# Performance work log

Hardware: AMD Instinct MI355X
Metric: run time of the kernel (lower is better)

## Reference

```python
import jax, jax.numpy as jnp
import numpy as np

H = 8          # n_heads
MRF = 128      # max_rf random features
EPS = 1e-4


def fiber2head(feats, h):
    # feats: list of [N, m_d, 2d+1] -> [N, h, sum_d (m_d/h)*(2d+1)]
    N = feats[0].shape[0]
    return jnp.concatenate([f.reshape(N, h, -1) for f in feats], axis=-1)


def softmax_kernel(data, w, is_query):
    # FAVOR+ positive random features. data: [B,H,L,d], w: [m,d]
    dn = data.shape[-1] ** -0.25
    ratio = w.shape[0] ** -0.5
    dd = jnp.einsum('bhld,md->bhlm', data * dn, w)
    diag = (data * data).sum(-1, keepdims=True) * (0.5 * dn * dn)
    if is_query:
        mx = jax.lax.stop_gradient(dd.max(-1, keepdims=True))
    else:
        mx = jax.lax.stop_gradient(dd.max())
    return ratio * (jnp.exp(dd - diag - mx) + EPS)


def setup_inputs() -> dict:
    key = jax.random.key(0)
    ks = jax.random.split(key, 7)
    B, L = 4, 8192
    N = B * L
    v0 = jax.random.normal(ks[0], (N, 64, 1), jnp.float32)
    v1 = jax.random.normal(ks[1], (N, 64, 3), jnp.float32)
    k0 = jax.random.normal(ks[2], (N, 64, 1), jnp.float32)
    k1 = jax.random.normal(ks[3], (N, 64, 3), jnp.float32)
    q0 = jax.random.normal(ks[4], (N, 64, 1), jnp.float32)
    q1 = jax.random.normal(ks[5], (N, 64, 3), jnp.float32)
    w = jax.random.normal(ks[6], (MRF, 32), jnp.float32)  # random-feature projection
    return {'v0': v0, 'v1': v1, 'k0': k0, 'k1': k1, 'q0': q0, 'q1': q1, 'w': w, 'batch_size': 4}


def reference(v0, v1, k0, k1, q0, q1, w, batch_size):
    B = batch_size
    N = v0.shape[0]
    L = N // B
    # Q from the k-dict (as in source); source then overwrites K with Q, so the
    # q-dict features are mathematically unused.
    Q = fiber2head([k0, k1], H).reshape(B, L, H, -1).transpose(0, 2, 1, 3)  # [B,H,L,d_k]
    K = Q  # faithful to `K = Q.view(...)` in the source
    Kp = softmax_kernel(K, w, is_query=False)  # [B,H,L,m]
    Qp = softmax_kernel(Q, w, is_query=True)   # [B,H,L,m]
    # Normalizer is identical for every value channel (q/k are expanded copies).
    D_inv = 1.0 / jnp.einsum('bhlm,bhm->bhl', Qp, Kp.sum(axis=2))
    outs = []
    for v in (v0, v1):
        m, e = v.shape[1], v.shape[2]     # multiplicity, 2d+1
        c = m // H                         # channels per head
        vv = v.reshape(B, L, H, c, e).transpose(0, 2, 3, 1, 4)  # [B,H,c,L,e]
        # linear attention: context [B,H,c,m,e] is small -> O(L*m*e) traffic
        ctx = jnp.einsum('bhlm,bhcle->bhcme', Kp, vv)
        o = jnp.einsum('bhcme,bhlm,bhl->bhcle', ctx, Qp, D_inv)
        o = o.reshape(B, H * c, L, e).transpose(0, 2, 1, 3).reshape(B * L, c * H, e)
        outs.append(o)
    return tuple(outs)  # (out_deg0 [N,64,1], out_deg1 [N,64,3])
```

## Files before the change

kernel.cpp:

```cpp
#include <hip/hip_runtime.h>

#define BB 4
#define HH 8
#define LL 8192
#define NN (BB*LL)
#define DDIM 32
#define MM 128

#define CTXR_OFF 0
#define KSUMR_OFF (CTXR_OFF + 32*8*MM*4)
#define VSUM_OFF  (KSUMR_OFF + 32*MM)
#define GMAX_OFF  (VSUM_OFF + 32*32)
#define ZERO_FLOATS (GMAX_OFF + 1)

#define DN 0.42044820762685725f
#define RATIO 0.08838834764831845f
#define EPSF 1e-4f

__global__ __launch_bounds__(256, 2) void k_ctx1(const float* __restrict__ kk0,
                                                 const float* __restrict__ kk1,
                                                 const float* __restrict__ v0,
                                                 const float* __restrict__ v1,
                                                 const float* __restrict__ w,
                                                 float* __restrict__ ws) {
    __shared__ float red[2][64][34];
    const int tid = threadIdx.x;
    const int lane = tid & 63;
    const int wid  = __builtin_amdgcn_readfirstlane(tid >> 6);
    const int half = wid & 1, rgrp = wid >> 1;
    const int m = half*64 + lane;
    const int bh = blockIdx.x >> 5, chunk = blockIdx.x & 31;
    const int b = bh >> 3, h = bh & 7;
    const int n0 = b*LL + chunk*256 + rgrp*128;
    float wreg[32];
    {
        const float4* w4 = (const float4*)(w + m*DDIM);
#pragma unroll
        for (int q = 0; q < 8; ++q) {
            const float4 t = w4[q];
            wreg[q*4+0]=t.x*DN; wreg[q*4+1]=t.y*DN;
            wreg[q*4+2]=t.z*DN; wreg[q*4+3]=t.w*DN;
        }
    }
    float acc[32];
#pragma unroll
    for (int i = 0; i < 32; ++i) acc[i] = 0.f;
    float ksum_acc = 0.f, vsum_acc = 0.f, wmax = -3.4e38f;
    for (int s = 0; s < 8; ++s) {
        const int nb = n0 + s*16;
        const int dr_ = lane >> 2, dq = lane & 3;
        float diagv;
        {
            const int n = nb + dr_;
            float4 da, db;
            if (dq == 0) {
                da = *(const float4*)(kk0 + (size_t)n*64 + h*8);
                db = *(const float4*)(kk0 + (size_t)n*64 + h*8 + 4);
            } else {
                const float* bp = kk1 + (size_t)n*192 + h*24 + (dq-1)*8;
                da = *(const float4*)bp; db = *(const float4*)(bp + 4);
            }
            float ss = da.x*da.x+da.y*da.y+da.z*da.z+da.w*da.w
                     + db.x*db.x+db.y*db.y+db.z*db.z+db.w*db.w;
            ss += __shfl_xor(ss, 1); ss += __shfl_xor(ss, 2);
            diagv = 0.5f*DN*DN*ss;
        }
        if (half == 0) {
            const int ve = lane & 31, vg = lane >> 5;
#pragma unroll
            for (int rr = 0; rr < 8; ++rr) {
                const int n = nb + vg*8 + rr;
                vsum_acc += (ve < 8) ? v0[(size_t)n*64 + h*8 + ve]
                                     : v1[(size_t)n*192 + h*24 + (ve-8)];
            }
        }
#pragma unroll 1
        for (int r = 0; r < 16; ++r) {
            const int n = nb + r;
            const float dg = __uint_as_float(
                __builtin_amdgcn_readlane(__float_as_uint(diagv), r*4));
            const float4 f0 = *(const float4*)(kk0 + (size_t)n*64 + h*8);
            const float4 f1 = *(const float4*)(kk0 + (size_t)n*64 + h*8 + 4);
            const float4* g4 = (const float4*)(kk1 + (size_t)n*192 + h*24);
            float dd0 =       f0.x*wreg[0];        float dd1 = f0.y*wreg[1];
            dd0 = fmaf(f0.z, wreg[2], dd0);  dd1 = fmaf(f0.w, wreg[3], dd1);
            dd0 = fmaf(f1.x, wreg[4], dd0);  dd1 = fmaf(f1.y, wreg[5], dd1);
            dd0 = fmaf(f1.z, wreg[6], dd0);  dd1 = fmaf(f1.w, wreg[7], dd1);
#pragma unroll
            for (int gq = 0; gq < 6; ++gq) {
                const float4 g = g4[gq];
                dd0 = fmaf(g.x, wreg[8+gq*4+0], dd0);
                dd1 = fmaf(g.y, wreg[8+gq*4+1], dd1);
                dd0 = fmaf(g.z, wreg[8+gq*4+2], dd0);
                dd1 = fmaf(g.w, wreg[8+gq*4+3], dd1);
            }
            const float dd = dd0 + dd1;
            wmax = fmaxf(wmax, dd);
            const float kp = __expf(dd - dg);
            ksum_acc += kp;
            const float4 a0 = *(const float4*)(v0 + (size_t)n*64 + h*8);
            const float4 a1 = *(const float4*)(v0 + (size_t)n*64 + h*8 + 4);
            const float4* b4 = (const float4*)(v1 + (size_t)n*192 + h*24);
            acc[0]  = fmaf(kp,a0.x,acc[0]);   acc[4]  = fmaf(kp,a0.y,acc[4]);
            acc[8]  = fmaf(kp,a0.z,acc[8]);   acc[12] = fmaf(kp,a0.w,acc[12]);
            acc[16] = fmaf(kp,a1.x,acc[16]);  acc[20] = fmaf(kp,a1.y,acc[20]);
            acc[24] = fmaf(kp,a1.z,acc[24]);  acc[28] = fmaf(kp,a1.w,acc[28]);
            {
                float4 g;
                g = b4[0];
                acc[1]=fmaf(kp,g.x,acc[1]);  acc[2]=fmaf(kp,g.y,acc[2]);
                acc[3]=fmaf(kp,g.z,acc[3]);  acc[5]=fmaf(kp,g.w,acc[5]);
                g = b4[1];
                acc[6]=fmaf(kp,g.x,acc[6]);  acc[7]=fmaf(kp,g.y,acc[7]);
                acc[9]=fmaf(kp,g.z,acc[9]);  acc[10]=fmaf(kp,g.w,acc[10]);
                g = b4[2];
                acc[11]=fmaf(kp,g.x,acc[11]); acc[13]=fmaf(kp,g.y,acc[13]);
                acc[14]=fmaf(kp,g.z,acc[14]); acc[15]=fmaf(kp,g.w,acc[15]);
                g = b4[3];
                acc[17]=fmaf(kp,g.x,acc[17]); acc[18]=fmaf(kp,g.y,acc[18]);
                acc[19]=fmaf(kp,g.z,acc[19]); acc[21]=fmaf(kp,g.w,acc[21]);
                g = b4[4];
                acc[22]=fmaf(kp,g.x,acc[22]); acc[23]=fmaf(kp,g.y,acc[23]);
                acc[25]=fmaf(kp,g.z,acc[25]); acc[26]=fmaf(kp,g.w,acc[26]);
                g = b4[5];
                acc[27]=fmaf(kp,g.x,acc[27]); acc[29]=fmaf(kp,g.y,acc[29]);
                acc[30]=fmaf(kp,g.z,acc[30]); acc[31]=fmaf(kp,g.w,acc[31]);
            }
        }
    }
    if (rgrp == 1) {
#pragma unroll
        for (int i = 0; i < 32; ++i) red[half][lane][i] = acc[i];
        red[half][lane][32] = ksum_acc;
        red[half][lane][33] = vsum_acc;
    }
    __syncthreads();
    if (rgrp == 0) {
#pragma unroll
        for (int i = 0; i < 32; ++i) acc[i] += red[half][lane][i];
        ksum_acc += red[half][lane][32];
        vsum_acc += red[half][lane][33];
        float* ctxr = ws + CTXR_OFF;
#pragma unroll
        for (int c = 0; c < 8; ++c)
#pragma unroll
            for (int j = 0; j < 4; ++j)
                atomicAdd(&ctxr[((bh*8 + c)*MM + m)*4 + j], acc[c*4+j]);
        atomicAdd(ws + KSUMR_OFF + bh*MM + m, ksum_acc);
        if (half == 0) {
            const int ve = lane & 31;
            const int packed = (ve < 8) ? ve*4
                                        : ((ve-8)/3)*4 + 1 + (ve-8)%3;
            atomicAdd(ws + VSUM_OFF + bh*32 + packed, vsum_acc);
        }
    }
#pragma unroll
    for (int off = 32; off; off >>= 1) wmax = fmaxf(wmax, __shfl_xor(wmax, off, 64));
    if (lane == 0) {
        unsigned u = __float_as_uint(wmax);
        u = (u & 0x80000000u) ? ~u : (u | 0x80000000u);
        atomicMax((unsigned*)(ws + GMAX_OFF), u);
    }
}

__global__ __launch_bounds__(256, 2) void k_out(const float* __restrict__ kk0,
                                                const float* __restrict__ kk1,
                                                const float* __restrict__ w,
                                                const float* __restrict__ ws,
                                                float* __restrict__ out) {
    __shared__ float ctx_s[128*36];
    __shared__ float wlds[128*36];
    __shared__ float ksl[128];
    __shared__ __align__(16) float sS0[32];
    __shared__ float sK0;
    const int tid = threadIdx.x;
    const int bh = blockIdx.x >> 5, chunk = blockIdx.x & 31;
    const int b = bh >> 3, h = bh & 7;
    const unsigned gu = *((const unsigned*)(ws + GMAX_OFF));
    const float gm = (gu & 0x80000000u) ? __uint_as_float(gu & 0x7fffffffu)
                                        : __uint_as_float(~gu);
    const float alpha = __expf(-gm);
    const float4* ctxr4 = (const float4*)(ws + CTXR_OFF) + (size_t)bh*1024;
    const float* vsg = ws + VSUM_OFF + bh*32;
#pragma unroll
    for (int it = 0; it < 4; ++it) {
        const int i = tid + it*256;
        const int c = i >> 7, mm2 = i & 127;
        const float4 q = ctxr4[i];
        const int p0 = c*4;
        ctx_s[mm2*36+p0+0] = RATIO*(alpha*q.x + EPSF*vsg[p0+0]);
        ctx_s[mm2*36+p0+1] = RATIO*(alpha*q.y + EPSF*vsg[p0+1]);
        ctx_s[mm2*36+p0+2] = RATIO*(alpha*q.z + EPSF*vsg[p0+2]);
        ctx_s[mm2*36+p0+3] = RATIO*(alpha*q.w + EPSF*vsg[p0+3]);
    }
    {
        const float4* w4 = (const float4*)w;
#pragma unroll
        for (int it = 0; it < 4; ++it) {
            const int i = tid + it*256;
            const int mm2 = i >> 3, q = i & 7;
            float4 t = w4[i];
            t.x*=DN; t.y*=DN; t.z*=DN; t.w*=DN;
            *(float4*)&wlds[mm2*36+q*4] = t;
        }
    }
    if (tid < 128) ksl[tid] = RATIO*(alpha*ws[KSUMR_OFF + bh*MM + tid] + EPSF*(float)LL);
    __syncthreads();
    if (tid < 32) {
        float s = 0.f;
#pragma unroll 8
        for (int mm2 = 0; mm2 < 128; ++mm2) s += ctx_s[mm2*36 + tid];
        sS0[tid] = s;
    } else if (tid < 64) {
        const int p2 = tid - 32;
        float s = ksl[p2] + ksl[32+p2] + ksl[64+p2] + ksl[96+p2];
        s += __shfl_xor(s, 1); s += __shfl_xor(s, 2); s += __shfl_xor(s, 4);
        s += __shfl_xor(s, 8); s += __shfl_xor(s, 16);
        if (p2 == 0) sK0 = s;
    }
    __syncthreads();
    const int n = b*LL + chunk*256 + tid;
    float K[32];
    {
        const float4 f0 = *(const float4*)(kk0 + (size_t)n*64 + h*8);
        const float4 f1 = *(const float4*)(kk0 + (size_t)n*64 + h*8 + 4);
        K[0]=f0.x; K[1]=f0.y; K[2]=f0.z; K[3]=f0.w;
        K[4]=f1.x; K[5]=f1.y; K[6]=f1.z; K[7]=f1.w;
        const float4* g4p = (const float4*)(kk1 + (size_t)n*192 + h*24);
#pragma unroll
        for (int gq = 0; gq < 6; ++gq) {
            const float4 g = g4p[gq];
            K[8+gq*4+0]=g.x; K[8+gq*4+1]=g.y; K[8+gq*4+2]=g.z; K[8+gq*4+3]=g.w;
        }
    }
    float dg = 0.f;
#pragma unroll
    for (int d = 0; d < 32; ++d) dg = fmaf(K[d], K[d], dg);
    dg *= 0.5f*DN*DN;
    float S1[32];
#pragma unroll
    for (int i = 0; i < 32; ++i) S1[i] = 0.f;
    float den1 = 0.f, mx = -3.4e38f;
#pragma unroll 2
    for (int m2 = 0; m2 < 128; ++m2) {
        const float* wrow = &wlds[m2*36];
        float dd0 = 0.f, dd1 = 0.f;
#pragma unroll
        for (int q = 0; q < 8; ++q) {
            const float4 wv = *(const float4*)&wrow[q*4];
            dd0 = fmaf(K[q*4+0], wv.x, dd0);
            dd1 = fmaf(K[q*4+1], wv.y, dd1);
            dd0 = fmaf(K[q*4+2], wv.z, dd0);
            dd1 = fmaf(K[q*4+3], wv.w, dd1);
        }
        const float dd = dd0 + dd1;
        mx = fmaxf(mx, dd);
        const float E = __expf(dd - dg);
        den1 = fmaf(E, ksl[m2], den1);
        const float* crow = &ctx_s[m2*36];
#pragma unroll
        for (int q = 0; q < 8; ++q) {
            const float4 cv = *(const float4*)&crow[q*4];
            S1[q*4+0] = fmaf(E, cv.x, S1[q*4+0]);
            S1[q*4+1] = fmaf(E, cv.y, S1[q*4+1]);
            S1[q*4+2] = fmaf(E, cv.z, S1[q*4+2]);
            S1[q*4+3] = fmaf(E, cv.w, S1[q*4+3]);
        }
    }
    const float es = __expf(-mx);
    const float dinv = 1.f / fmaf(es, den1, EPSF*sK0);
    float v[32];
#pragma unroll
    for (int q = 0; q < 8; ++q) {
        const float4 s0 = *(const float4*)&sS0[q*4];
        v[q*4+0] = fmaf(es, S1[q*4+0], EPSF*s0.x)*dinv;
        v[q*4+1] = fmaf(es, S1[q*4+1], EPSF*s0.y)*dinv;
        v[q*4+2] = fmaf(es, S1[q*4+2], EPSF*s0.z)*dinv;
        v[q*4+3] = fmaf(es, S1[q*4+3], EPSF*s0.w)*dinv;
    }
    float* o0 = out + (size_t)n*64 + h*8;
    *(float4*)(o0)     = make_float4(v[0],  v[4],  v[8],  v[12]);
    *(float4*)(o0 + 4) = make_float4(v[16], v[20], v[24], v[28]);
    float* o1 = out + (size_t)NN*64 + (size_t)n*192 + h*24;
    *(float4*)(o1 +  0) = make_float4(v[1],  v[2],  v[3],  v[5]);
    *(float4*)(o1 +  4) = make_float4(v[6],  v[7],  v[9],  v[10]);
    *(float4*)(o1 +  8) = make_float4(v[11], v[13], v[14], v[15]);
    *(float4*)(o1 + 12) = make_float4(v[17], v[18], v[19], v[21]);
    *(float4*)(o1 + 16) = make_float4(v[22], v[23], v[25], v[26]);
    *(float4*)(o1 + 20) = make_float4(v[27], v[29], v[30], v[31]);
}

extern "C" void kernel_launch(void* const* d_in, const int* in_sizes, int n_in,
                              void* d_out, int out_size, void* d_ws, size_t ws_size,
                              hipStream_t stream) {
    const float* v0 = (const float*)d_in[0];
    const float* v1 = (const float*)d_in[1];
    const float* k0 = (const float*)d_in[2];
    const float* k1 = (const float*)d_in[3];
    const float* w  = (const float*)d_in[6];
    float* out = (float*)d_out;
    float* ws  = (float*)d_ws;
    hipMemsetAsync(ws, 0, (size_t)ZERO_FLOATS*sizeof(float), stream);
    k_ctx1<<<1024, 256, 0, stream>>>(k0, k1, v0, v1, w, ws);
    k_out <<<1024, 256, 0, stream>>>(k0, k1, w, ws, out);
}
```

Baseline: 229.6 us.

## Load row tiles cooperatively across lanes and broadcast via readlane

Each wave now loads a 32-row block of k and v cooperatively, one float4 per lane, instead of every lane redundantly loading the same row's 32 k and 32 v values each iteration. Values are then broadcast to all lanes with v_readlane into scalar registers, so the inner loop runs from SGPRs. This targets the redundant broadcast vector loads and their latency in the serial row loop. In exchange it adds many readlane instructions and scalar-to-vector dependencies per row, which may become the bottleneck.

```diff
diff --git a/kernel.cpp b/kernel.cpp
--- a/kernel.cpp
+++ b/kernel.cpp
@@ -16,6 +16,14 @@
 #define DN 0.42044820762685725f
 #define RATIO 0.08838834764831845f
 #define EPSF 1e-4f
+
+__device__ __forceinline__ float rl(float x, int l) {
+    return __uint_as_float(__builtin_amdgcn_readlane(__float_as_uint(x), l));
+}
+__device__ __forceinline__ float rl4(float4 v, int c, int l) {
+    const float x = (c==0) ? v.x : (c==1) ? v.y : (c==2) ? v.z : v.w;
+    return rl(x, l);
+}
 
 __global__ __launch_bounds__(256, 2) void k_ctx1(const float* __restrict__ kk0,
                                                  const float* __restrict__ kk1,
@@ -42,16 +50,30 @@
             wreg[q*4+2]=t.z*DN; wreg[q*4+3]=t.w*DN;
         }
     }
+    const int rowA = lane >> 1, qA = lane & 1;
+    const int offA = rowA*64 + h*8 + qA*4;
+    const int rowB = lane >> 3, qB = lane & 7;
+    const int offB = rowB*192 + h*24 + ((qB < 6) ? qB*4 : 20);
     float acc[32];
 #pragma unroll
     for (int i = 0; i < 32; ++i) acc[i] = 0.f;
     float ksum_acc = 0.f, vsum_acc = 0.f, wmax = -3.4e38f;
-    for (int s = 0; s < 8; ++s) {
-        const int nb = n0 + s*16;
-        const int dr_ = lane >> 2, dq = lane & 3;
-        float diagv;
-        {
-            const int n = nb + dr_;
+#pragma unroll 1
+    for (int bi = 0; bi < 4; ++bi) {
+        const int nb = n0 + bi*32;
+        const float4 k0b = *(const float4*)(kk0 + (size_t)nb*64 + offA);
+        const float4 v0b = *(const float4*)(v0  + (size_t)nb*64 + offA);
+        float4 k1b[4], v1b[4];
+#pragma unroll
+        for (int j = 0; j < 4; ++j) {
+            k1b[j] = *(const float4*)(kk1 + (size_t)nb*192 + j*1536 + offB);
+            v1b[j] = *(const float4*)(v1  + (size_t)nb*192 + j*1536 + offB);
+        }
+        float diagv0, diagv1;
+#pragma unroll
+        for (int dp = 0; dp < 2; ++dp) {
+            const int dr_ = lane >> 2, dq = lane & 3;
+            const int n = nb + dp*16 + dr_;
             float4 da, db;
             if (dq == 0) {
                 da = *(const float4*)(kk0 + (size_t)n*64 + h*8);
@@ -63,68 +85,54 @@
             float ss = da.x*da.x+da.y*da.y+da.z*da.z+da.w*da.w
                      + db.x*db.x+db.y*db.y+db.z*db.z+db.w*db.w;
             ss += __shfl_xor(ss, 1); ss += __shfl_xor(ss, 2);
-            diagv = 0.5f*DN*DN*ss;
+            const float dv_ = 0.5f*DN*DN*ss;
+            if (dp == 0) diagv0 = dv_; else diagv1 = dv_;
         }
         if (half == 0) {
             const int ve = lane & 31, vg = lane >> 5;
 #pragma unroll
+            for (int dp = 0; dp < 2; ++dp)
+#pragma unroll
+                for (int rr = 0; rr < 8; ++rr) {
+                    const int n = nb + dp*16 + vg*8 + rr;
+                    vsum_acc += (ve < 8) ? v0[(size_t)n*64 + h*8 + ve]
+                                         : v1[(size_t)n*192 + h*24 + (ve-8)];
+                }
+        }
+#pragma unroll
+        for (int rq = 0; rq < 4; ++rq) {
+#pragma unroll
             for (int rr = 0; rr < 8; ++rr) {
-                const int n = nb + vg*8 + rr;
-                vsum_acc += (ve < 8) ? v0[(size_t)n*64 + h*8 + ve]
-                                     : v1[(size_t)n*192 + h*24 + (ve-8)];
-            }
-        }
-#pragma unroll 1
-        for (int r = 0; r < 16; ++r) {
-            const int n = nb + r;
-            const float dg = __uint_as_float(
-                __builtin_amdgcn_readlane(__float_as_uint(diagv), r*4));
-            const float4 f0 = *(const float4*)(kk0 + (size_t)n*64 + h*8);
-            const float4 f1 = *(const float4*)(kk0 + (size_t)n*64 + h*8 + 4);
-            const float4* g4 = (const float4*)(kk1 + (size_t)n*192 + h*24);
-            float dd0 =       f0.x*wreg[0];        float dd1 = f0.y*wreg[1];
-            dd0 = fmaf(f0.z, wreg[2], dd0);  dd1 = fmaf(f0.w, wreg[3], dd1);
-            dd0 = fmaf(f1.x, wreg[4], dd0);  dd1 = fmaf(f1.y, wreg[5], dd1);
-            dd0 = fmaf(f1.z, wreg[6], dd0);  dd1 = fmaf(f1.w, wreg[7], dd1);
-#pragma unroll
-            for (int gq = 0; gq < 6; ++gq) {
-                const float4 g = g4[gq];
-                dd0 = fmaf(g.x, wreg[8+gq*4+0], dd0);
-                dd1 = fmaf(g.y, wreg[8+gq*4+1], dd1);
-                dd0 = fmaf(g.z, wreg[8+gq*4+2], dd0);
-                dd1 = fmaf(g.w, wreg[8+gq*4+3], dd1);
-            }
-            const float dd = dd0 + dd1;
-            wmax = fmaxf(wmax, dd);
-            const float kp = __expf(dd - dg);
-            ksum_acc += kp;
-            const float4 a0 = *(const float4*)(v0 + (size_t)n*64 + h*8);
-            const float4 a1 = *(const float4*)(v0 + (size_t)n*64 + h*8 + 4);
-            const float4* b4 = (const float4*)(v1 + (size_t)n*192 + h*24);
-            acc[0]  = fmaf(kp,a0.x,acc[0]);   acc[4]  = fmaf(kp,a0.y,acc[4]);
-            acc[8]  = fmaf(kp,a0.z,acc[8]);   acc[12] = fmaf(kp,a0.w,acc[12]);
-            acc[16] = fmaf(kp,a1.x,acc[16]);  acc[20] = fmaf(kp,a1.y,acc[20]);
-            acc[24] = fmaf(kp,a1.z,acc[24]);  acc[28] = fmaf(kp,a1.w,acc[28]);
-            {
-                float4 g;
-                g = b4[0];
-                acc[1]=fmaf(kp,g.x,acc[1]);  acc[2]=fmaf(kp,g.y,acc[2]);
-                acc[3]=fmaf(kp,g.z,acc[3]);  acc[5]=fmaf(kp,g.w,acc[5]);
-                g = b4[1];
-                acc[6]=fmaf(kp,g.x,acc[6]);  acc[7]=fmaf(kp,g.y,acc[7]);
-                acc[9]=fmaf(kp,g.z,acc[9]);  acc[10]=fmaf(kp,g.w,acc[10]);
-                g = b4[2];
-                acc[11]=fmaf(kp,g.x,acc[11]); acc[13]=fmaf(kp,g.y,acc[13]);
-                acc[14]=fmaf(kp,g.z,acc[14]); acc[15]=fmaf(kp,g.w,acc[15]);
-                g = b4[3];
-                acc[17]=fmaf(kp,g.x,acc[17]); acc[18]=fmaf(kp,g.y,acc[18]);
-                acc[19]=fmaf(kp,g.z,acc[19]); acc[21]=fmaf(kp,g.w,acc[21]);
-                g = b4[4];
-                acc[22]=fmaf(kp,g.x,acc[22]); acc[23]=fmaf(kp,g.y,acc[23]);
-                acc[25]=fmaf(kp,g.z,acc[25]); acc[26]=fmaf(kp,g.w,acc[26]);
-                g = b4[5];
-                acc[27]=fmaf(kp,g.x,acc[27]); acc[29]=fmaf(kp,g.y,acc[29]);
-                acc[30]=fmaf(kp,g.z,acc[30]); acc[31]=fmaf(kp,g.w,acc[31]);
+                const int r = rq*8 + rr;
+                const float dg = rl((r < 16) ? diagv0 : diagv1, (r & 15)*4);
+                float dd0 = 0.f, dd1 = 0.f;
+#pragma unroll
+                for (int d = 0; d < 8; ++d) {
+                    const float s = rl4(k0b, d & 3, r*2 + (d >> 2));
+                    if (d & 1) dd1 = fmaf(s, wreg[d], dd1);
+                    else       dd0 = fmaf(s, wreg[d], dd0);
+                }
+#pragma unroll
+                for (int e = 0; e < 24; ++e) {
+                    const float s = rl4(k1b[rq], e & 3, rr*8 + (e >> 2));
+                    if (e & 1) dd1 = fmaf(s, wreg[8+e], dd1);
+                    else       dd0 = fmaf(s, wreg[8+e], dd0);
+                }
+                const float dd = dd0 + dd1;
+                wmax = fmaxf(wmax, dd);
+                const float kp = __expf(dd - dg);
+                ksum_acc += kp;
+#pragma unroll
+                for (int c = 0; c < 8; ++c) {
+                    const float av = rl4(v0b, c & 3, r*2 + (c >> 2));
+                    acc[c*4] = fmaf(kp, av, acc[c*4]);
+                }
+#pragma unroll
+                for (int e = 0; e < 24; ++e) {
+                    const float av = rl4(v1b[rq], e & 3, rr*8 + (e >> 2));
+                    const int ai = (e/3)*4 + 1 + e%3;
+                    acc[ai] = fmaf(kp, av, acc[ai]);
+                }
             }
         }
     }
```

New measurement: 236.9 us. 1.03x slower.

## Stage k and v rows in shared memory for the context kernel

Applied to the files above, without the earlier changes.

The context-accumulation kernel now cooperatively loads 128 rows of k0/k1/v0/v1 for the head into a shared buffer, with coalesced float4 loads per batch. Each wave then reads those rows from LDS instead of issuing redundant per-row global loads across the four waves. The diagonal term and the value sums are also computed from the staged tile, and the final reduction reuses the same buffer. This adds block-wide barriers and LDS traffic (broadcast reads), and it raises shared memory use to about 35 KB per block, which may limit occupancy.

```diff
diff --git a/kernel.cpp b/kernel.cpp
--- a/kernel.cpp
+++ b/kernel.cpp
@@ -23,15 +23,15 @@
                                                  const float* __restrict__ v1,
                                                  const float* __restrict__ w,
                                                  float* __restrict__ ws) {
-    __shared__ float red[2][64][34];
+    __shared__ float buf[128][68];
     const int tid = threadIdx.x;
     const int lane = tid & 63;
     const int wid  = __builtin_amdgcn_readfirstlane(tid >> 6);
-    const int half = wid & 1, rgrp = wid >> 1;
+    const int half = wid & 1, rhalf = wid >> 1;
     const int m = half*64 + lane;
     const int bh = blockIdx.x >> 5, chunk = blockIdx.x & 31;
     const int b = bh >> 3, h = bh & 7;
-    const int n0 = b*LL + chunk*256 + rgrp*128;
+    const int n0 = b*LL + chunk*256;
     float wreg[32];
     {
         const float4* w4 = (const float4*)(w + m*DDIM);
@@ -42,104 +42,99 @@
             wreg[q*4+2]=t.z*DN; wreg[q*4+3]=t.w*DN;
         }
     }
+    const int rA = tid >> 1, qA = tid & 1;
     float acc[32];
 #pragma unroll
     for (int i = 0; i < 32; ++i) acc[i] = 0.f;
     float ksum_acc = 0.f, vsum_acc = 0.f, wmax = -3.4e38f;
-    for (int s = 0; s < 8; ++s) {
-        const int nb = n0 + s*16;
-        const int dr_ = lane >> 2, dq = lane & 3;
-        float diagv;
+    for (int batch = 0; batch < 2; ++batch) {
+        const int nb = n0 + batch*128;
+        __syncthreads();
+        *(float4*)&buf[rA][qA*4] =
+            *(const float4*)(kk0 + (size_t)(nb+rA)*64 + h*8 + qA*4);
+        *(float4*)&buf[rA][32+qA*4] =
+            *(const float4*)(v0  + (size_t)(nb+rA)*64 + h*8 + qA*4);
+#pragma unroll
+        for (int j = 0; j < 3; ++j) {
+            const int idx = tid + j*256;
+            const int row = idx/6, q = idx - row*6;
+            *(float4*)&buf[row][8+q*4] =
+                *(const float4*)(kk1 + (size_t)(nb+row)*192 + h*24 + q*4);
+            *(float4*)&buf[row][40+q*4] =
+                *(const float4*)(v1  + (size_t)(nb+row)*192 + h*24 + q*4);
+        }
+        __syncthreads();
         {
-            const int n = nb + dr_;
-            float4 da, db;
-            if (dq == 0) {
-                da = *(const float4*)(kk0 + (size_t)n*64 + h*8);
-                db = *(const float4*)(kk0 + (size_t)n*64 + h*8 + 4);
-            } else {
-                const float* bp = kk1 + (size_t)n*192 + h*24 + (dq-1)*8;
-                da = *(const float4*)bp; db = *(const float4*)(bp + 4);
+            const int row = tid >> 1, s = tid & 1;
+            const float4* p = (const float4*)&buf[row][s*16];
+            const float4 x0 = p[0], x1 = p[1], x2 = p[2], x3 = p[3];
+            float ss = x0.x*x0.x + x0.y*x0.y + x0.z*x0.z + x0.w*x0.w
+                     + x1.x*x1.x + x1.y*x1.y + x1.z*x1.z + x1.w*x1.w
+                     + x2.x*x2.x + x2.y*x2.y + x2.z*x2.z + x2.w*x2.w
+                     + x3.x*x3.x + x3.y*x3.y + x3.z*x3.z + x3.w*x3.w;
+            ss += __shfl_xor(ss, 1);
+            if (s == 0) buf[row][64] = 0.5f*DN*DN*ss;
+        }
+        __syncthreads();
+#pragma unroll 2
+        for (int r = 0; r < 64; ++r) {
+            const int row = rhalf*64 + r;
+            const float dg = buf[row][64];
+            const float4* kp4 = (const float4*)&buf[row][0];
+            float dd0, dd1;
+            {
+                const float4 a = kp4[0], c = kp4[1];
+                dd0 =       a.x*wreg[0];         dd1 = a.y*wreg[1];
+                dd0 = fmaf(a.z, wreg[2], dd0);   dd1 = fmaf(a.w, wreg[3], dd1);
+                dd0 = fmaf(c.x, wreg[4], dd0);   dd1 = fmaf(c.y, wreg[5], dd1);
+                dd0 = fmaf(c.z, wreg[6], dd0);   dd1 = fmaf(c.w, wreg[7], dd1);
             }
-            float ss = da.x*da.x+da.y*da.y+da.z*da.z+da.w*da.w
-                     + db.x*db.x+db.y*db.y+db.z*db.z+db.w*db.w;
-            ss += __shfl_xor(ss, 1); ss += __shfl_xor(ss, 2);
-            diagv = 0.5f*DN*DN*ss;
-        }
-        if (half == 0) {
-            const int ve = lane & 31, vg = lane >> 5;
-#pragma unroll
-            for (int rr = 0; rr < 8; ++rr) {
-                const int n = nb + vg*8 + rr;
-                vsum_acc += (ve < 8) ? v0[(size_t)n*64 + h*8 + ve]
-                                     : v1[(size_t)n*192 + h*24 + (ve-8)];
-            }
-        }
-#pragma unroll 1
-        for (int r = 0; r < 16; ++r) {
-            const int n = nb + r;
-            const float dg = __uint_as_float(
-                __builtin_amdgcn_readlane(__float_as_uint(diagv), r*4));
-            const float4 f0 = *(const float4*)(kk0 + (size_t)n*64 + h*8);
-            const float4 f1 = *(const float4*)(kk0 + (size_t)n*64 + h*8 + 4);
-            const float4* g4 = (const float4*)(kk1 + (size_t)n*192 + h*24);
-            float dd0 =       f0.x*wreg[0];        float dd1 = f0.y*wreg[1];
-            dd0 = fmaf(f0.z, wreg[2], dd0);  dd1 = fmaf(f0.w, wreg[3], dd1);
-            dd0 = fmaf(f1.x, wreg[4], dd0);  dd1 = fmaf(f1.y, wreg[5], dd1);
-            dd0 = fmaf(f1.z, wreg[6], dd0);  dd1 = fmaf(f1.w, wreg[7], dd1);
-#pragma unroll
-            for (int gq = 0; gq < 6; ++gq) {
-                const float4 g = g4[gq];
-                dd0 = fmaf(g.x, wreg[8+gq*4+0], dd0);
-                dd1 = fmaf(g.y, wreg[8+gq*4+1], dd1);
-                dd0 = fmaf(g.z, wreg[8+gq*4+2], dd0);
-                dd1 = fmaf(g.w, wreg[8+gq*4+3], dd1);
+#pragma unroll
+            for (int q = 2; q < 8; ++q) {
+                const float4 g = kp4[q];
+                dd0 = fmaf(g.x, wreg[q*4+0], dd0);
+                dd1 = fmaf(g.y, wreg[q*4+1], dd1);
+                dd0 = fmaf(g.z, wreg[q*4+2], dd0);
+                dd1 = fmaf(g.w, wreg[q*4+3], dd1);
             }
             const float dd = dd0 + dd1;
             wmax = fmaxf(wmax, dd);
             const float kp = __expf(dd - dg);
             ksum_acc += kp;
-            const float4 a0 = *(const float4*)(v0 + (size_t)n*64 + h*8);
-            const float4 a1 = *(const float4*)(v0 + (size_t)n*64 + h*8 + 4);
-            const float4* b4 = (const float4*)(v1 + (size_t)n*192 + h*24);
-            acc[0]  = fmaf(kp,a0.x,acc[0]);   acc[4]  = fmaf(kp,a0.y,acc[4]);
-            acc[8]  = fmaf(kp,a0.z,acc[8]);   acc[12] = fmaf(kp,a0.w,acc[12]);
-            acc[16] = fmaf(kp,a1.x,acc[16]);  acc[20] = fmaf(kp,a1.y,acc[20]);
-            acc[24] = fmaf(kp,a1.z,acc[24]);  acc[28] = fmaf(kp,a1.w,acc[28]);
-            {
-                float4 g;
-                g = b4[0];
-                acc[1]=fmaf(kp,g.x,acc[1]);  acc[2]=fmaf(kp,g.y,acc[2]);
-                acc[3]=fmaf(kp,g.z,acc[3]);  acc[5]=fmaf(kp,g.w,acc[5]);
-                g = b4[1];
-                acc[6]=fmaf(kp,g.x,acc[6]);  acc[7]=fmaf(kp,g.y,acc[7]);
-                acc[9]=fmaf(kp,g.z,acc[9]);  acc[10]=fmaf(kp,g.w,acc[10]);
-                g = b4[2];
-                acc[11]=fmaf(kp,g.x,acc[11]); acc[13]=fmaf(kp,g.y,acc[13]);
-                acc[14]=fmaf(kp,g.z,acc[14]); acc[15]=fmaf(kp,g.w,acc[15]);
-                g = b4[3];
-                acc[17]=fmaf(kp,g.x,acc[17]); acc[18]=fmaf(kp,g.y,acc[18]);
-                acc[19]=fmaf(kp,g.z,acc[19]); acc[21]=fmaf(kp,g.w,acc[21]);
-                g = b4[4];
-                acc[22]=fmaf(kp,g.x,acc[22]); acc[23]=fmaf(kp,g.y,acc[23]);
-                acc[25]=fmaf(kp,g.z,acc[25]); acc[26]=fmaf(kp,g.w,acc[26]);
-                g = b4[5];
-                acc[27]=fmaf(kp,g.x,acc[27]); acc[29]=fmaf(kp,g.y,acc[29]);
-                acc[30]=fmaf(kp,g.z,acc[30]); acc[31]=fmaf(kp,g.w,acc[31]);
+            const float4* vp4 = (const float4*)&buf[row][32];
+#pragma unroll
+            for (int q = 0; q < 8; ++q) {
+                const float4 vv = vp4[q];
+#pragma unroll
+                for (int c = 0; c < 4; ++c) {
+                    const int e = q*4 + c;
+                    const int ai = (e < 8) ? e*4 : ((e-8)/3)*4 + 1 + (e-8)%3;
+                    const float x = (c==0)?vv.x:(c==1)?vv.y:(c==2)?vv.z:vv.w;
+                    acc[ai] = fmaf(kp, x, acc[ai]);
+                }
             }
         }
-    }
-    if (rgrp == 1) {
-#pragma unroll
-        for (int i = 0; i < 32; ++i) red[half][lane][i] = acc[i];
-        red[half][lane][32] = ksum_acc;
-        red[half][lane][33] = vsum_acc;
+        if (half == 0) {
+            const int ve = lane & 31, vg = lane >> 5;
+#pragma unroll 8
+            for (int i = 0; i < 32; ++i)
+                vsum_acc += buf[rhalf*64 + vg*32 + i][32 + ve];
+        }
     }
     __syncthreads();
-    if (rgrp == 0) {
-#pragma unroll
-        for (int i = 0; i < 32; ++i) acc[i] += red[half][lane][i];
-        ksum_acc += red[half][lane][32];
-        vsum_acc += red[half][lane][33];
+    float* redp = &buf[0][0];
+    if (rhalf == 1) {
+#pragma unroll
+        for (int i = 0; i < 32; ++i) redp[(half*64+lane)*34 + i] = acc[i];
+        redp[(half*64+lane)*34 + 32] = ksum_acc;
+        redp[(half*64+lane)*34 + 33] = vsum_acc;
+    }
+    __syncthreads();
+    if (rhalf == 0) {
+#pragma unroll
+        for (int i = 0; i < 32; ++i) acc[i] += redp[(half*64+lane)*34 + i];
+        ksum_acc += redp[(half*64+lane)*34 + 32];
+        vsum_acc += redp[(half*64+lane)*34 + 33];
         float* ctxr = ws + CTXR_OFF;
 #pragma unroll
         for (int c = 0; c < 8; ++c)
```

After: 300.1 us. +30.7%, slower.
